# Kernel tuning notes

Hardware: AMD Instinct MI355X
Metric: run time of the kernel (lower is better)

The kernel has to match this reference:

```python
import jax, jax.numpy as jnp
import numpy as np

E, B, D, T = 8, 4096, 2048, 2048
H = D // 2 + T // 2  # expert hidden dim = 2048
TOP_K = 2


def setup_inputs() -> dict:
    key = jax.random.key(0)
    ks = jax.random.split(key, 5)
    s_in = 1.0 / np.sqrt(D)
    s_h = 1.0 / np.sqrt(H)
    return {
        "xs": jax.random.normal(ks[0], (E, B, D), dtype=jnp.float32),
        "Wg": jax.random.normal(ks[1], (D,), dtype=jnp.float32) * s_in,
        "bg": jnp.zeros((1,), dtype=jnp.float32),
        "W1": jax.random.normal(ks[2], (E, D, H), dtype=jnp.float32) * s_in,
        "b1": jnp.zeros((E, H), dtype=jnp.float32),
        "W2": jax.random.normal(ks[3], (E, H, T), dtype=jnp.float32) * s_h,
        "b2": jnp.zeros((E, T), dtype=jnp.float32),
    }


def reference(xs, Wg, bg, W1, b1, W2, b2):
    # Gating: logits[b, e] = x[e][b] @ Wg + bg  -> [B, E]
    logits = jnp.einsum("ebd,d->be", xs, Wg) + bg
    probs = jax.nn.softmax(logits, axis=1)
    top_k_values, top_k_indices = jax.lax.top_k(probs, TOP_K)  # [B, K]

    # Dense expert compute over each expert's own input stream.
    # hidden[e, b, h] = relu(x[e] @ W1[e] + b1[e]); out[e, b, t] = hidden @ W2[e] + b2[e]
    hidden = jax.nn.relu(jnp.einsum("ebd,edh->ebh", xs, W1) + b1[:, None, :])
    expert_out = jnp.einsum("ebh,eht->ebt", hidden, W2) + b2[:, None, :]  # [E, B, T]

    # Gather the top-k experts per token. In the original, masked-dense compute
    # + output mask is mathematically identical to this gather.
    per_token = jnp.transpose(expert_out, (1, 0, 2))  # [B, E, T]
    selected = jnp.take_along_axis(per_token, top_k_indices[:, :, None], axis=1)  # [B, K, T]

    out = jnp.sum(top_k_values[:, :, None] * selected, axis=1)  # [B, T]
    return out, top_k_values
```

## Files before the change

kernel.cpp:

```cpp
#include <hip/hip_runtime.h>
#include <hip/hip_bf16.h>
#include <stdint.h>

#define E_ 8
#define B_ 4096
#define D_ 2048
#define T_ 2048
#define H_ 2048
#define KDIM 2048
#define NDIM 2048
#define ECAP 2048
#define NROWS (E_ * 1024 + 256)

typedef __attribute__((ext_vector_type(4))) float f32x4;
typedef __attribute__((ext_vector_type(8))) unsigned short u16x8;
typedef __attribute__((ext_vector_type(8))) __bf16 bf16x8;

__device__ __forceinline__ unsigned short f2bf(float f) {
    __hip_bfloat16 h = __float2bfloat16(f);
    return __builtin_bit_cast(unsigned short, h);
}

__device__ __forceinline__ void gload_lds16(const void* g, void* lds) {
    __builtin_amdgcn_global_load_lds(
        (const __attribute__((address_space(1))) void*)g,
        (__attribute__((address_space(3))) void*)lds, 16, 0, 0);
}

__global__ __launch_bounds__(256) void fused_pre(
    const float* __restrict__ xs, const float* __restrict__ Wg,
    const float* __restrict__ bg,
    const float* __restrict__ W1, const float* __restrict__ W2,
    unsigned short* __restrict__ Wt1, unsigned short* __restrict__ Wt2,
    float* __restrict__ out_topk, int* __restrict__ counts,
    unsigned short* __restrict__ Axf, int* __restrict__ tokf,
    float* __restrict__ probf, int nwt)
{
    const int bid = blockIdx.x;
    const int t = threadIdx.x;

    if (bid < nwt) {
        const int z   = bid >> 10;
        const int rem = bid & 1023;
        const int kb  = ((rem >> 5) & 31) << 6;
        const int nb  = (rem & 31) << 6;
        const int e   = z & 7;
        const float* W = (z >> 3) ? W2 : W1;
        unsigned short* Wt = (z >> 3) ? Wt2 : Wt1;

        __shared__ float tile[64][68];
        const float* src = W + ((size_t)e * KDIM + kb) * NDIM + nb;
        {
            const int kr = t >> 2, nc = (t & 3) * 16;
            #pragma unroll
            for (int j = 0; j < 4; ++j) {
                f32x4 v = __builtin_nontemporal_load(
                    (const f32x4*)(src + (size_t)kr * NDIM + nc + j * 4));
                *(f32x4*)&tile[kr][nc + j * 4] = v;
            }
        }
        __syncthreads();
        {
            const int nn = t >> 2, kc = (t & 3) * 16;
            unsigned short wbuf[16];
            #pragma unroll
            for (int j = 0; j < 16; ++j) wbuf[j] = f2bf(tile[kc + j][nn]);
            unsigned short* dst =
                Wt + ((size_t)e * NDIM + nb + nn) * KDIM + kb + kc;
            *(u16x8*)dst       = *(const u16x8*)&wbuf[0];
            *((u16x8*)dst + 1) = *(const u16x8*)&wbuf[8];
        }
        return;
    }

    const int b = bid - nwt;
    const int wave = t >> 6, lane = t & 63;
    __shared__ float red[E_][4];
    __shared__ int sh_i0, sh_i1, sh_p0, sh_p1;

    const f32x4 wg0 = ((const f32x4*)Wg)[t];
    const f32x4 wg1 = ((const f32x4*)Wg)[t + 256];

    f32x4 xa[E_], xb[E_];
    #pragma unroll
    for (int e = 0; e < E_; ++e) {
        const f32x4* xr = (const f32x4*)(xs + ((size_t)e * B_ + b) * D_);
        xa[e] = __builtin_nontemporal_load(&xr[t]);
        xb[e] = __builtin_nontemporal_load(&xr[t + 256]);
        float p = xa[e].x*wg0.x + xa[e].y*wg0.y + xa[e].z*wg0.z + xa[e].w*wg0.w
                + xb[e].x*wg1.x + xb[e].y*wg1.y + xb[e].z*wg1.z + xb[e].w*wg1.w;
        #pragma unroll
        for (int off = 32; off >= 1; off >>= 1) p += __shfl_xor(p, off);
        if (lane == 0) red[e][wave] = p;
    }
    __syncthreads();
    if (t == 0) {
        float pr[E_];
        float mx = -3.0e38f;
        #pragma unroll
        for (int e = 0; e < E_; ++e) {
            pr[e] = red[e][0] + red[e][1] + red[e][2] + red[e][3] + bg[0];
            mx = fmaxf(mx, pr[e]);
        }
        float s = 0.f;
        #pragma unroll
        for (int e = 0; e < E_; ++e) { pr[e] = expf(pr[e] - mx); s += pr[e]; }
        float inv = 1.0f / s;
        #pragma unroll
        for (int e = 0; e < E_; ++e) pr[e] *= inv;
        int i0 = 0;
        #pragma unroll
        for (int e = 1; e < E_; ++e) if (pr[e] > pr[i0]) i0 = e;
        int i1 = (i0 == 0) ? 1 : 0;
        #pragma unroll
        for (int e = 0; e < E_; ++e) { if (e != i0 && pr[e] > pr[i1]) i1 = e; }
        float p0 = pr[i0], p1 = pr[i1];
        out_topk[2*b]   = p0;
        out_topk[2*b+1] = p1;
        int pos0 = atomicAdd(&counts[i0], 1);
        int pos1 = atomicAdd(&counts[i1], 1);
        if (pos0 >= ECAP) pos0 = ECAP - 1;
        if (pos1 >= ECAP) pos1 = ECAP - 1;
        tokf[i0 * ECAP + pos0] = b;  probf[i0 * ECAP + pos0] = p0;
        tokf[i1 * ECAP + pos1] = b;  probf[i1 * ECAP + pos1] = p1;
        sh_i0 = i0; sh_i1 = i1; sh_p0 = pos0; sh_p1 = pos1;
    }
    __syncthreads();
    const int i0 = sh_i0, i1 = sh_i1;
    f32x4 s0a = xa[0], s0b = xb[0], s1a = xa[0], s1b = xb[0];
    #pragma unroll
    for (int e = 0; e < E_; ++e) {
        if (i0 == e) { s0a = xa[e]; s0b = xb[e]; }
        if (i1 == e) { s1a = xa[e]; s1b = xb[e]; }
    }
    unsigned short* r0 = Axf + (size_t)(i0 * ECAP + sh_p0) * D_;
    unsigned short* r1 = Axf + (size_t)(i1 * ECAP + sh_p1) * D_;
    r0[4*t+0]=f2bf(s0a.x); r0[4*t+1]=f2bf(s0a.y); r0[4*t+2]=f2bf(s0a.z); r0[4*t+3]=f2bf(s0a.w);
    r0[1024+4*t+0]=f2bf(s0b.x); r0[1024+4*t+1]=f2bf(s0b.y); r0[1024+4*t+2]=f2bf(s0b.z); r0[1024+4*t+3]=f2bf(s0b.w);
    r1[4*t+0]=f2bf(s1a.x); r1[4*t+1]=f2bf(s1a.y); r1[4*t+2]=f2bf(s1a.z); r1[4*t+3]=f2bf(s1a.w);
    r1[1024+4*t+0]=f2bf(s1b.x); r1[1024+4*t+1]=f2bf(s1b.y); r1[1024+4*t+2]=f2bf(s1b.z); r1[1024+4*t+3]=f2bf(s1b.w);
}

__global__ void build_tiles(const int* __restrict__ counts,
                            int* __restrict__ tiles, int* __restrict__ ebase)
{
    if (threadIdx.x == 0 && blockIdx.x == 0) {
        int n = 0, base = 0;
        for (int e = 0; e < E_; ++e) {
            ebase[e] = base;
            int c = counts[e]; if (c > ECAP) c = ECAP;
            int te = (c + 255) >> 8;
            for (int m = 0; m < te; ++m) tiles[1 + n++] = (e << 16) | m;
            base += c;
        }
        tiles[0] = n;
    }
}

__global__ __launch_bounds__(256) void wtrans1(
    const float* __restrict__ W, unsigned short* __restrict__ Wt)
{
    const int e  = blockIdx.z;
    const int kb = blockIdx.x * 64;
    const int nb = blockIdx.y * 64;
    const int t  = threadIdx.x;
    __shared__ float tile[64][68];

    const float* src = W + ((size_t)e * KDIM + kb) * NDIM + nb;
    {
        const int kr = t >> 2, nc = (t & 3) * 16;
        #pragma unroll
        for (int j = 0; j < 4; ++j) {
            f32x4 v = __builtin_nontemporal_load(
                (const f32x4*)(src + (size_t)kr * NDIM + nc + j * 4));
            *(f32x4*)&tile[kr][nc + j * 4] = v;
        }
    }
    __syncthreads();
    {
        const int nn = t >> 2, kc = (t & 3) * 16;
        unsigned short wbuf[16];
        #pragma unroll
        for (int j = 0; j < 16; ++j) wbuf[j] = f2bf(tile[kc + j][nn]);
        unsigned short* dst = Wt + ((size_t)e * NDIM + nb + nn) * KDIM + kb + kc;
        *(u16x8*)dst       = *(const u16x8*)&wbuf[0];
        *((u16x8*)dst + 1) = *(const u16x8*)&wbuf[8];
    }
}

#define BAR  __builtin_amdgcn_s_barrier()

template<int LAYER>
__global__ __launch_bounds__(1024, 4) void moe_gemm(
    const unsigned short* __restrict__ Abuf,
    const unsigned short* __restrict__ Wt,
    const float* __restrict__ bias,
    const int* __restrict__ counts,
    const int* __restrict__ tiles,
    const int* __restrict__ ebase,
    const int* __restrict__ tokf,
    const float* __restrict__ probf,
    unsigned short* __restrict__ hidden_out,
    float* __restrict__ out)
{
    const int nMt = tiles[0];
    const int bid = blockIdx.x;
    const int mt  = bid >> 3;
    const int np  = bid & 7;
    if (mt >= nMt) return;
    const int info = tiles[1 + mt];
    const int e    = info >> 16;
    const int mloc = (info & 0xffff) * 256;
    const int arow0 = (LAYER == 1) ? (e * ECAP + mloc) : (ebase[e] + mloc);
    const int n0   = np * 256;
    int n_e = counts[e]; if (n_e > ECAP) n_e = ECAP;

    const int t = threadIdx.x;
    const int lane = t & 63;
    const int w = t >> 6;
    const int wm = (w >> 2) * 64;
    const int wn = (w & 3) * 64;
    const int lg = lane >> 4;

    __shared__ u16x8 As[4 * 1024];
    __shared__ u16x8 Bs[4 * 1024];

    const int ksw = (((t & 3) ^ ((t >> 3) & 3)) << 3);
    const unsigned short* aptr = Abuf + (size_t)(arow0 + (t >> 2)) * KDIM + ksw;
    const unsigned short* bptr =
        Wt + ((size_t)e * NDIM + n0 + (t >> 2)) * KDIM + ksw;

#define STG(BUF, KT) do{ \
    gload_lds16(aptr + (KT)*32, &As[(BUF)*1024 + w*64]); \
    gload_lds16(bptr + (KT)*32, &Bs[(BUF)*1024 + w*64]); }while(0)

    f32x4 acc[4][4];
    #pragma unroll
    for (int i = 0; i < 4; ++i)
        #pragma unroll
        for (int j = 0; j < 4; ++j) {
            f32x4 z = {0.f, 0.f, 0.f, 0.f};
            acc[i][j] = z;
        }

    STG(0, 0); STG(1, 1); STG(2, 2);

    const int usw = (lane >> 1) & 3;
    for (int kt = 0; kt < 64; ++kt) {
        asm volatile("s_waitcnt vmcnt(4)" ::: "memory");
        BAR;
        int tn = kt + 3; if (tn > 63) tn = 63;
        STG((kt + 3) & 3, tn);

        const int base = (kt & 3) * 1024;
        bf16x8 af[4];
        #pragma unroll
        for (int mi = 0; mi < 4; ++mi) {
            const int row = wm + mi * 16 + (lane & 15);
            af[mi] = __builtin_bit_cast(bf16x8, As[base + row * 4 + (lg ^ usw)]);
        }
        #pragma unroll
        for (int ni = 0; ni < 4; ++ni) {
            const int row = wn + ni * 16 + (lane & 15);
            bf16x8 bq = __builtin_bit_cast(bf16x8, Bs[base + row * 4 + (lg ^ usw)]);
            #pragma unroll
            for (int mi = 0; mi < 4; ++mi)
                acc[mi][ni] = __builtin_amdgcn_mfma_f32_16x16x32_bf16(
                    af[mi], bq, acc[mi][ni], 0, 0, 0);
        }
    }
    asm volatile("s_waitcnt vmcnt(0)" ::: "memory");

    #pragma unroll
    for (int mi = 0; mi < 4; ++mi) {
        #pragma unroll
        for (int rr = 0; rr < 4; ++rr) {
            const int rloc = wm + mi * 16 + ((lane >> 4) << 2) + rr;
            if (mloc + rloc >= n_e) continue;
            #pragma unroll
            for (int ni = 0; ni < 4; ++ni) {
                const int col = n0 + wn + ni * 16 + (lane & 15);
                float v = acc[mi][ni][rr];
                if (LAYER == 1) {
                    v += bias[e * NDIM + col];
                    v = fmaxf(v, 0.f);
                    hidden_out[(size_t)(ebase[e] + mloc + rloc) * H_ + col] = f2bf(v);
                } else {
                    const int f = e * ECAP + mloc + rloc;
                    v = (v + bias[e * NDIM + col]) * probf[f];
                    atomicAdd(&out[(size_t)tokf[f] * T_ + col], v);
                }
            }
        }
    }
#undef STG
}

extern "C" void kernel_launch(void* const* d_in, const int* in_sizes, int n_in,
                              void* d_out, int out_size, void* d_ws, size_t ws_size,
                              hipStream_t stream)
{
    const float* xs = (const float*)d_in[0];
    const float* Wg = (const float*)d_in[1];
    const float* bg = (const float*)d_in[2];
    const float* W1 = (const float*)d_in[3];
    const float* b1 = (const float*)d_in[4];
    const float* W2 = (const float*)d_in[5];
    const float* b2 = (const float*)d_in[6];

    float* out      = (float*)d_out;
    float* out_topk = out + (size_t)B_ * T_;

    char* ws = (char*)d_ws;
    int*   counts = (int*)ws;
    int*   tiles  = (int*)(ws + 256);
    int*   ebase  = (int*)(ws + 768);
    int*   tokf   = (int*)(ws + 1024);
    float* probf  = (float*)(ws + 1024 + E_ * ECAP * 4);
    size_t off = 1024 + (size_t)E_ * ECAP * 8;
    off = (off + 255) & ~(size_t)255;
    unsigned short* Axf    = (unsigned short*)(ws + off); off += (size_t)E_ * ECAP * D_ * 2;
    unsigned short* hidden = (unsigned short*)(ws + off); off += (size_t)NROWS * H_ * 2;
    unsigned short* Wt1    = (unsigned short*)(ws + off); off += (size_t)E_ * KDIM * NDIM * 2;
    size_t off_big = off + (size_t)E_ * KDIM * NDIM * 2;
    unsigned short* Wt2 = (unsigned short*)(ws + off);

    const bool big = (ws_size >= off_big);

    hipMemsetAsync(counts, 0, 256, stream);
    hipMemsetAsync(out, 0, (size_t)B_ * T_ * sizeof(float), stream);

    dim3 blk(256), gblk(1024);
    dim3 ggrid(39 * 8);

    if (big) {
        const int nwt = 16 * 1024;
        fused_pre<<<dim3(nwt + B_), blk, 0, stream>>>(
            xs, Wg, bg, W1, W2, Wt1, Wt2, out_topk, counts, Axf, tokf, probf, nwt);
        build_tiles<<<dim3(1), dim3(64), 0, stream>>>(counts, tiles, ebase);
        moe_gemm<1><<<ggrid, gblk, 0, stream>>>(
            Axf, Wt1, b1, counts, tiles, ebase, tokf, probf, hidden, nullptr);
        moe_gemm<2><<<ggrid, gblk, 0, stream>>>(
            hidden, Wt2, b2, counts, tiles, ebase, tokf, probf, nullptr, out);
    } else {
        dim3 tgrid(32, 32, E_);
        fused_pre<<<dim3(B_), blk, 0, stream>>>(
            xs, Wg, bg, W1, W2, Wt1, Wt1, out_topk, counts, Axf, tokf, probf, 0);
        build_tiles<<<dim3(1), dim3(64), 0, stream>>>(counts, tiles, ebase);
        wtrans1<<<tgrid, blk, 0, stream>>>(W1, Wt1);
        moe_gemm<1><<<ggrid, gblk, 0, stream>>>(
            Axf, Wt1, b1, counts, tiles, ebase, tokf, probf, hidden, nullptr);
        wtrans1<<<tgrid, blk, 0, stream>>>(W2, Wt1);
        moe_gemm<2><<<ggrid, gblk, 0, stream>>>(
            hidden, Wt1, b2, counts, tiles, ebase, tokf, probf, nullptr, out);
    }
}
```

Measured before the change: 498.9 us.

## Drop build_tiles launch, compute tile map in GEMM, pad transpose tile, vectorize stores

```diff
diff --git a/kernel.cpp b/kernel.cpp
--- a/kernel.cpp
+++ b/kernel.cpp
@@ -10,9 +10,9 @@
 #define KDIM 2048
 #define NDIM 2048
 #define ECAP 2048
-#define NROWS (E_ * 1024 + 256)
 
 typedef __attribute__((ext_vector_type(4))) float f32x4;
+typedef __attribute__((ext_vector_type(4))) unsigned short u16x4;
 typedef __attribute__((ext_vector_type(8))) unsigned short u16x8;
 typedef __attribute__((ext_vector_type(8))) __bf16 bf16x8;
 
@@ -48,7 +48,7 @@
         const float* W = (z >> 3) ? W2 : W1;
         unsigned short* Wt = (z >> 3) ? Wt2 : Wt1;
 
-        __shared__ float tile[64][68];
+        __shared__ float tile[64][65];
         const float* src = W + ((size_t)e * KDIM + kb) * NDIM + nb;
         {
             const int kr = t >> 2, nc = (t & 3) * 16;
@@ -56,7 +56,10 @@
             for (int j = 0; j < 4; ++j) {
                 f32x4 v = __builtin_nontemporal_load(
                     (const f32x4*)(src + (size_t)kr * NDIM + nc + j * 4));
-                *(f32x4*)&tile[kr][nc + j * 4] = v;
+                tile[kr][nc + j*4 + 0] = v.x;
+                tile[kr][nc + j*4 + 1] = v.y;
+                tile[kr][nc + j*4 + 2] = v.z;
+                tile[kr][nc + j*4 + 3] = v.w;
             }
         }
         __syncthreads();
@@ -135,26 +138,15 @@
     }
     unsigned short* r0 = Axf + (size_t)(i0 * ECAP + sh_p0) * D_;
     unsigned short* r1 = Axf + (size_t)(i1 * ECAP + sh_p1) * D_;
-    r0[4*t+0]=f2bf(s0a.x); r0[4*t+1]=f2bf(s0a.y); r0[4*t+2]=f2bf(s0a.z); r0[4*t+3]=f2bf(s0a.w);
-    r0[1024+4*t+0]=f2bf(s0b.x); r0[1024+4*t+1]=f2bf(s0b.y); r0[1024+4*t+2]=f2bf(s0b.z); r0[1024+4*t+3]=f2bf(s0b.w);
-    r1[4*t+0]=f2bf(s1a.x); r1[4*t+1]=f2bf(s1a.y); r1[4*t+2]=f2bf(s1a.z); r1[4*t+3]=f2bf(s1a.w);
-    r1[1024+4*t+0]=f2bf(s1b.x); r1[1024+4*t+1]=f2bf(s1b.y); r1[1024+4*t+2]=f2bf(s1b.z); r1[1024+4*t+3]=f2bf(s1b.w);
-}
-
-__global__ void build_tiles(const int* __restrict__ counts,
-                            int* __restrict__ tiles, int* __restrict__ ebase)
-{
-    if (threadIdx.x == 0 && blockIdx.x == 0) {
-        int n = 0, base = 0;
-        for (int e = 0; e < E_; ++e) {
-            ebase[e] = base;
-            int c = counts[e]; if (c > ECAP) c = ECAP;
-            int te = (c + 255) >> 8;
-            for (int m = 0; m < te; ++m) tiles[1 + n++] = (e << 16) | m;
-            base += c;
-        }
-        tiles[0] = n;
-    }
+    u16x4 w;
+    w[0]=f2bf(s0a.x); w[1]=f2bf(s0a.y); w[2]=f2bf(s0a.z); w[3]=f2bf(s0a.w);
+    *(u16x4*)(r0 + 4*t) = w;
+    w[0]=f2bf(s0b.x); w[1]=f2bf(s0b.y); w[2]=f2bf(s0b.z); w[3]=f2bf(s0b.w);
+    *(u16x4*)(r0 + 1024 + 4*t) = w;
+    w[0]=f2bf(s1a.x); w[1]=f2bf(s1a.y); w[2]=f2bf(s1a.z); w[3]=f2bf(s1a.w);
+    *(u16x4*)(r1 + 4*t) = w;
+    w[0]=f2bf(s1b.x); w[1]=f2bf(s1b.y); w[2]=f2bf(s1b.z); w[3]=f2bf(s1b.w);
+    *(u16x4*)(r1 + 1024 + 4*t) = w;
 }
 
 __global__ __launch_bounds__(256) void wtrans1(
@@ -164,7 +156,7 @@
     const int kb = blockIdx.x * 64;
     const int nb = blockIdx.y * 64;
     const int t  = threadIdx.x;
-    __shared__ float tile[64][68];
+    __shared__ float tile[64][65];
 
     const float* src = W + ((size_t)e * KDIM + kb) * NDIM + nb;
     {
@@ -173,7 +165,10 @@
         for (int j = 0; j < 4; ++j) {
             f32x4 v = __builtin_nontemporal_load(
                 (const f32x4*)(src + (size_t)kr * NDIM + nc + j * 4));
-            *(f32x4*)&tile[kr][nc + j * 4] = v;
+            tile[kr][nc + j*4 + 0] = v.x;
+            tile[kr][nc + j*4 + 1] = v.y;
+            tile[kr][nc + j*4 + 2] = v.z;
+            tile[kr][nc + j*4 + 3] = v.w;
         }
     }
     __syncthreads();
@@ -196,24 +191,31 @@
     const unsigned short* __restrict__ Wt,
     const float* __restrict__ bias,
     const int* __restrict__ counts,
-    const int* __restrict__ tiles,
-    const int* __restrict__ ebase,
     const int* __restrict__ tokf,
     const float* __restrict__ probf,
     unsigned short* __restrict__ hidden_out,
     float* __restrict__ out)
 {
-    const int nMt = tiles[0];
     const int bid = blockIdx.x;
     const int mt  = bid >> 3;
     const int np  = bid & 7;
+
+    int nMt = 0, base = 0;
+    int e = -1, mloc = 0, eb = 0, n_e = 0;
+    #pragma unroll
+    for (int ee = 0; ee < E_; ++ee) {
+        int ce = counts[ee]; if (ce > ECAP) ce = ECAP;
+        int te = (ce + 255) >> 8;
+        if (e < 0 && mt < nMt + te) {
+            e = ee; mloc = (mt - nMt) * 256; eb = base; n_e = ce;
+        }
+        nMt += te;
+        base += ce;
+    }
     if (mt >= nMt) return;
-    const int info = tiles[1 + mt];
-    const int e    = info >> 16;
-    const int mloc = (info & 0xffff) * 256;
-    const int arow0 = (LAYER == 1) ? (e * ECAP + mloc) : (ebase[e] + mloc);
-    const int n0   = np * 256;
-    int n_e = counts[e]; if (n_e > ECAP) n_e = ECAP;
+
+    const int arow0 = (LAYER == 1) ? (e * ECAP + mloc) : (eb + mloc);
+    const int n0 = np * 256;
 
     const int t = threadIdx.x;
     const int lane = t & 63;
@@ -252,17 +254,17 @@
         int tn = kt + 3; if (tn > 63) tn = 63;
         STG((kt + 3) & 3, tn);
 
-        const int base = (kt & 3) * 1024;
+        const int bse = (kt & 3) * 1024;
         bf16x8 af[4];
         #pragma unroll
         for (int mi = 0; mi < 4; ++mi) {
             const int row = wm + mi * 16 + (lane & 15);
-            af[mi] = __builtin_bit_cast(bf16x8, As[base + row * 4 + (lg ^ usw)]);
+            af[mi] = __builtin_bit_cast(bf16x8, As[bse + row * 4 + (lg ^ usw)]);
         }
         #pragma unroll
         for (int ni = 0; ni < 4; ++ni) {
             const int row = wn + ni * 16 + (lane & 15);
-            bf16x8 bq = __builtin_bit_cast(bf16x8, Bs[base + row * 4 + (lg ^ usw)]);
+            bf16x8 bq = __builtin_bit_cast(bf16x8, Bs[bse + row * 4 + (lg ^ usw)]);
             #pragma unroll
             for (int mi = 0; mi < 4; ++mi)
                 acc[mi][ni] = __builtin_amdgcn_mfma_f32_16x16x32_bf16(
@@ -284,7 +286,7 @@
                 if (LAYER == 1) {
                     v += bias[e * NDIM + col];
                     v = fmaxf(v, 0.f);
-                    hidden_out[(size_t)(ebase[e] + mloc + rloc) * H_ + col] = f2bf(v);
+                    hidden_out[(size_t)(eb + mloc + rloc) * H_ + col] = f2bf(v);
                 } else {
                     const int f = e * ECAP + mloc + rloc;
                     v = (v + bias[e * NDIM + col]) * probf[f];
@@ -313,14 +315,12 @@
 
     char* ws = (char*)d_ws;
     int*   counts = (int*)ws;
-    int*   tiles  = (int*)(ws + 256);
-    int*   ebase  = (int*)(ws + 768);
     int*   tokf   = (int*)(ws + 1024);
     float* probf  = (float*)(ws + 1024 + E_ * ECAP * 4);
     size_t off = 1024 + (size_t)E_ * ECAP * 8;
     off = (off + 255) & ~(size_t)255;
     unsigned short* Axf    = (unsigned short*)(ws + off); off += (size_t)E_ * ECAP * D_ * 2;
-    unsigned short* hidden = (unsigned short*)(ws + off); off += (size_t)NROWS * H_ * 2;
+    unsigned short* hidden = (unsigned short*)(ws + off); off += (size_t)(2 * B_ + 256) * H_ * 2;
     unsigned short* Wt1    = (unsigned short*)(ws + off); off += (size_t)E_ * KDIM * NDIM * 2;
     size_t off_big = off + (size_t)E_ * KDIM * NDIM * 2;
     unsigned short* Wt2 = (unsigned short*)(ws + off);
@@ -337,21 +337,19 @@
         const int nwt = 16 * 1024;
         fused_pre<<<dim3(nwt + B_), blk, 0, stream>>>(
             xs, Wg, bg, W1, W2, Wt1, Wt2, out_topk, counts, Axf, tokf, probf, nwt);
-        build_tiles<<<dim3(1), dim3(64), 0, stream>>>(counts, tiles, ebase);
         moe_gemm<1><<<ggrid, gblk, 0, stream>>>(
-            Axf, Wt1, b1, counts, tiles, ebase, tokf, probf, hidden, nullptr);
+            Axf, Wt1, b1, counts, tokf, probf, hidden, nullptr);
         moe_gemm<2><<<ggrid, gblk, 0, stream>>>(
-            hidden, Wt2, b2, counts, tiles, ebase, tokf, probf, nullptr, out);
+            hidden, Wt2, b2, counts, tokf, probf, nullptr, out);
     } else {
         dim3 tgrid(32, 32, E_);
         fused_pre<<<dim3(B_), blk, 0, stream>>>(
             xs, Wg, bg, W1, W2, Wt1, Wt1, out_topk, counts, Axf, tokf, probf, 0);
-        build_tiles<<<dim3(1), dim3(64), 0, stream>>>(counts, tiles, ebase);
         wtrans1<<<tgrid, blk, 0, stream>>>(W1, Wt1);
         moe_gemm<1><<<ggrid, gblk, 0, stream>>>(
-            Axf, Wt1, b1, counts, tiles, ebase, tokf, probf, hidden, nullptr);
+            Axf, Wt1, b1, counts, tokf, probf, hidden, nullptr);
         wtrans1<<<tgrid, blk, 0, stream>>>(W2, Wt1);
         moe_gemm<2><<<ggrid, gblk, 0, stream>>>(
-            hidden, Wt1, b2, counts, tiles, ebase, tokf, probf, nullptr, out);
-    }
-}
+            hidden, Wt1, b2, counts, tokf, probf, nullptr, out);
+    }
+}
```

New measurement: 493.8 us. No clear change (-1.0%).
